# Kernel tuning notes

Hardware: AMD Instinct MI355X
Metric: run time of the kernel (lower is better)

The kernel has to match this reference:

```python
import jax, jax.numpy as jnp
import numpy as np


def setup_inputs() -> dict:
    key = jax.random.key(0)
    ks = jax.random.split(key, 8)
    B = 65536
    x = jax.random.normal(ks[0], (B, 784), dtype=jnp.float32)
    conv_w = jnp.ones((3, 3), dtype=jnp.float32)  # Parameter(ones((3,3)))
    # Linear layers stored as (in, out) weight + (out,) bias
    def lin(k, fin, fout):
        kw, kb = jax.random.split(k)
        bound = 1.0 / np.sqrt(fin)
        W = jax.random.uniform(kw, (fin, fout), minval=-bound, maxval=bound, dtype=jnp.float32)
        b = jax.random.uniform(kb, (fout,), minval=-bound, maxval=bound, dtype=jnp.float32)
        return W, b
    W1, b1 = lin(ks[1], 26 * 26, 500)
    W2, b2 = lin(ks[2], 500, 200)
    W3, b3 = lin(ks[3], 200, 10)
    return {"x": x, "conv_w": conv_w, "W1": W1, "b1": b1,
            "W2": W2, "b2": b2, "W3": W3, "b3": b3}


def reference(x, conv_w, W1, b1, W2, b2, W3, b3):
    B = x.shape[0]
    img = x.reshape(B, 1, 28, 28)  # NCHW, single channel
    kern = conv_w.reshape(1, 1, 3, 3)  # OIHW
    # valid 2D cross-correlation == torch tensordot sliding-window loop
    conv = jax.lax.conv_general_dilated(
        img, kern, window_strides=(1, 1), padding='VALID',
        dimension_numbers=('NCHW', 'OIHW', 'NCHW'))  # (B,1,26,26)
    h = conv.reshape(B, 26 * 26)
    h = jax.nn.relu(h @ W1 + b1)
    h = jax.nn.relu(h @ W2 + b2)
    return h @ W3 + b3  # (B, 10) logits
```

## Files before the change

### kernel.cpp

```cpp
#include <hip/hip_runtime.h>
#include <hip/hip_bf16.h>
#include <stdint.h>

typedef __bf16 bf16x8 __attribute__((ext_vector_type(8)));
typedef float  f32x4  __attribute__((ext_vector_type(4)));


#define KT1 25
#define NF1 32
#define KT2 16
#define NF2 16
#define KT3 8

__global__ void prep_w1(const float* __restrict__ W1, const float* __restrict__ cw,
                        __bf16* __restrict__ w1s) {
  int gid  = blockIdx.x * 256 + threadIdx.x;
  int lane = gid & 63;
  int slot = gid >> 6;
  int t = slot >> 5;
  int f = slot & 31;
  int kbase = t * 32 + ((lane >> 4) << 3);
  int n = f * 16 + (lane & 15);
  float c[9];
#pragma unroll
  for (int i = 0; i < 9; ++i) c[i] = cw[i];
  bf16x8 v;
#pragma unroll
  for (int e = 0; e < 8; ++e) {
    int k = kbase + e;
    float acc = 0.f;
    if (k < 784 && n < 500) {
      int pi = k / 28, pj = k % 28;
#pragma unroll
      for (int dr = 0; dr < 3; ++dr) {
        int r = pi - dr;
        if (r < 0 || r >= 26) continue;
#pragma unroll
        for (int dc = 0; dc < 3; ++dc) {
          int cc = pj - dc;
          if (cc < 0 || cc >= 26) continue;
          acc += c[dr * 3 + dc] * W1[(size_t)(r * 26 + cc) * 500 + n];
        }
      }
    }
    v[e] = (__bf16)acc;
  }
  *(bf16x8*)(w1s + (size_t)(slot * 64 + lane) * 8) = v;
}

__global__ void prep_w2(const float* __restrict__ W2, __bf16* __restrict__ w2s) {
  int gid  = blockIdx.x * 256 + threadIdx.x;
  int lane = gid & 63;
  int slot = gid >> 6;
  int t = slot >> 4;
  int f = slot & 15;
  int kbase = t * 32 + ((lane >> 4) << 3);
  int n = f * 16 + (lane & 15);
  bf16x8 v;
#pragma unroll
  for (int e = 0; e < 8; ++e) {
    int k = kbase + e;
    float val = (k < 500 && n < 200) ? W2[(size_t)k * 200 + n] : 0.f;
    v[e] = (__bf16)val;
  }
  *(bf16x8*)(w2s + (size_t)(slot * 64 + lane) * 8) = v;
}

__global__ void prep_w3(const float* __restrict__ W3, __bf16* __restrict__ w3s) {
  int gid  = blockIdx.x * 256 + threadIdx.x;
  int lane = gid & 63;
  int t    = gid >> 6;
  int kbase = t * 32 + ((lane >> 4) << 3);
  int n = lane & 15;
  bf16x8 v;
#pragma unroll
  for (int e = 0; e < 8; ++e) {
    int k = kbase + e;
    float val = (k < 200 && n < 10) ? W3[(size_t)k * 10 + n] : 0.f;
    v[e] = (__bf16)val;
  }
  *(bf16x8*)(w3s + (size_t)(t * 64 + lane) * 8) = v;
}

__global__ __launch_bounds__(256, 2) void mlp_fused(
    const float* __restrict__ x,
    const __bf16* __restrict__ w1s, const __bf16* __restrict__ w2s,
    const __bf16* __restrict__ w3s,
    const float* __restrict__ b1, const float* __restrict__ b2,
    const float* __restrict__ b3,
    float* __restrict__ out)
{
  __shared__ __align__(16) char xsm[2 * 4096];
  __shared__ __align__(16) char h1[64 * 1024];
  __shared__ float sb1[512];
  __shared__ float sb2[256];

  const int tid  = threadIdx.x;
  const int lane = tid & 63;
  const int w    = tid >> 6;
  const int lrow = lane & 15;
  const int lgrp = lane >> 4;
  const int brow = blockIdx.x * 64;
  const int xr   = tid >> 2;
  const int xq   = tid & 3;

  sb1[tid]       = (tid < 500) ? b1[tid] : 0.f;
  sb1[tid + 256] = (tid + 256 < 500) ? b1[tid + 256] : 0.f;
  sb2[tid]       = (tid < 200) ? b2[tid] : 0.f;

  const f32x4 FZ = {0.f, 0.f, 0.f, 0.f};

  f32x4 acc1[4][8];
#pragma unroll
  for (int m = 0; m < 4; ++m)
#pragma unroll
    for (int f = 0; f < 8; ++f) acc1[m][f] = FZ;

  const bf16x8* w1p   = (const bf16x8*)w1s + ((size_t)(w * 8) * 64 + lane);
  const float*  xbase = x + (size_t)(brow + xr) * 784;
  const int     xoff  = xr * 64 + ((xq ^ (xr & 3)) << 4);

  auto gload = [&](int t, f32x4 (&g)[2]) {
    int gk = t * 32 + xq * 8;
    if (gk > 776) gk = 776;
    const float* p = xbase + gk;
    g[0] = *(const f32x4*)p;
    g[1] = *(const f32x4*)(p + 4);
  };
  auto cwrite = [&](f32x4 (&g)[2], int bw) {
    bf16x8 v;
#pragma unroll
    for (int e = 0; e < 4; ++e) { v[e] = (__bf16)g[0][e]; v[e + 4] = (__bf16)g[1][e]; }
    *(bf16x8*)(xsm + bw + xoff) = v;
  };

  f32x4  grA[2], grB[2];
  bf16x8 bA[8], bB[8];

  auto body1 = [&](int t, bf16x8 (&bc)[8], bf16x8 (&bn)[8],
                   f32x4 (&gc)[2], f32x4 (&gl)[2], int bufR, int bufW) {
    bf16x8 afr[4];
#pragma unroll
    for (int m = 0; m < 4; ++m) {
      int r = m * 16 + lrow;
      afr[m] = *(const bf16x8*)(xsm + bufR + r * 64 + ((lgrp ^ (r & 3)) << 4));
    }
#pragma unroll
    for (int f = 0; f < 8; ++f) bn[f] = w1p[(size_t)((t + 1) * NF1 + f) * 64];
    gload(t + 2 > 24 ? 24 : t + 2, gl);
    cwrite(gc, bufW);

    __builtin_amdgcn_s_setprio(1);
#pragma unroll
    for (int f = 0; f < 8; ++f)
#pragma unroll
      for (int m = 0; m < 4; ++m)
        acc1[m][f] = __builtin_amdgcn_mfma_f32_16x16x32_bf16(afr[m], bc[f], acc1[m][f], 0, 0, 0);
    __builtin_amdgcn_s_setprio(0);

    asm volatile("s_waitcnt lgkmcnt(0)\n\ts_barrier" ::: "memory");
  };

  gload(0, grA);
#pragma unroll
  for (int f = 0; f < 8; ++f) bA[f] = w1p[(size_t)f * 64];
  gload(1, grB);
  cwrite(grA, 0);
  asm volatile("s_waitcnt lgkmcnt(0)\n\ts_barrier" ::: "memory");

  for (int t = 0; t < 24; t += 2) {
    body1(t,     bA, bB, grB, grA, 0,    4096);
    body1(t + 1, bB, bA, grA, grB, 4096, 0);
  }
  {
    bf16x8 afr[4];
#pragma unroll
    for (int m = 0; m < 4; ++m) {
      int r = m * 16 + lrow;
      afr[m] = *(const bf16x8*)(xsm + r * 64 + ((lgrp ^ (r & 3)) << 4));
    }
    __builtin_amdgcn_s_setprio(1);
#pragma unroll
    for (int f = 0; f < 8; ++f)
#pragma unroll
      for (int m = 0; m < 4; ++m)
        acc1[m][f] = __builtin_amdgcn_mfma_f32_16x16x32_bf16(afr[m], bA[f], acc1[m][f], 0, 0, 0);
    __builtin_amdgcn_s_setprio(0);
  }

#pragma unroll
  for (int m = 0; m < 4; ++m) {
#pragma unroll
    for (int f = 0; f < 8; ++f) {
      int col = w * 128 + f * 16 + lrow;
      float bias = sb1[col];
#pragma unroll
      for (int r = 0; r < 4; ++r) {
        int row = m * 16 + lgrp * 4 + r;
        float v = fmaxf(acc1[m][f][r] + bias, 0.f);
        int off = row * 1024 + ((col * 2) ^ ((row & 7) << 4));
        *(__bf16*)(h1 + off) = (__bf16)v;
      }
    }
  }

  const bf16x8* w2p = (const bf16x8*)w2s + ((size_t)(w * 4) * 64 + lane);
  bf16x8 bX[2][4], bY[2][4];
#pragma unroll
  for (int f = 0; f < 4; ++f) bX[0][f] = w2p[(size_t)(0 * NF2 + f) * 64];
#pragma unroll
  for (int f = 0; f < 4; ++f) bX[1][f] = w2p[(size_t)(1 * NF2 + f) * 64];

  asm volatile("s_waitcnt lgkmcnt(0)\n\ts_barrier" ::: "memory");

  f32x4 acc2[4][4];
#pragma unroll
  for (int m = 0; m < 4; ++m)
#pragma unroll
    for (int f = 0; f < 4; ++f) acc2[m][f] = FZ;

  auto pair2 = [&](int tt, bf16x8 (&cur)[2][4], bf16x8 (&nxt)[2][4]) {
#pragma unroll
    for (int f = 0; f < 4; ++f) nxt[0][f] = w2p[(size_t)((tt + 2) * NF2 + f) * 64];
#pragma unroll
    for (int f = 0; f < 4; ++f) nxt[1][f] = w2p[(size_t)((tt + 3) * NF2 + f) * 64];
    {
      bf16x8 a2[4];
#pragma unroll
      for (int m = 0; m < 4; ++m) {
        int row = m * 16 + lrow;
        int off = row * 1024 + ((tt * 64 + lgrp * 16) ^ ((row & 7) << 4));
        a2[m] = *(const bf16x8*)(h1 + off);
      }
      __builtin_amdgcn_s_setprio(1);
#pragma unroll
      for (int f = 0; f < 4; ++f)
#pragma unroll
        for (int m = 0; m < 4; ++m)
          acc2[m][f] = __builtin_amdgcn_mfma_f32_16x16x32_bf16(a2[m], cur[0][f], acc2[m][f], 0, 0, 0);
      __builtin_amdgcn_s_setprio(0);
    }
    {
      bf16x8 a2[4];
#pragma unroll
      for (int m = 0; m < 4; ++m) {
        int row = m * 16 + lrow;
        int off = row * 1024 + (((tt + 1) * 64 + lgrp * 16) ^ ((row & 7) << 4));
        a2[m] = *(const bf16x8*)(h1 + off);
      }
      __builtin_amdgcn_s_setprio(1);
#pragma unroll
      for (int f = 0; f < 4; ++f)
#pragma unroll
        for (int m = 0; m < 4; ++m)
          acc2[m][f] = __builtin_amdgcn_mfma_f32_16x16x32_bf16(a2[m], cur[1][f], acc2[m][f], 0, 0, 0);
      __builtin_amdgcn_s_setprio(0);
    }
  };

  for (int t = 0; t < KT2; t += 4) {
    pair2(t,     bX, bY);
    pair2(t + 2, bY, bX);
  }

  asm volatile("s_waitcnt lgkmcnt(0)\n\ts_barrier" ::: "memory");

#pragma unroll
  for (int m = 0; m < 4; ++m) {
#pragma unroll
    for (int f = 0; f < 4; ++f) {
      int col = w * 64 + f * 16 + lrow;
      float bias = sb2[col];
#pragma unroll
      for (int r = 0; r < 4; ++r) {
        int row = m * 16 + lgrp * 4 + r;
        float v = fmaxf(acc2[m][f][r] + bias, 0.f);
        int off = row * 512 + ((col * 2) ^ ((row & 7) << 4));
        *(__bf16*)(h1 + off) = (__bf16)v;
      }
    }
  }

  const bf16x8* w3p = (const bf16x8*)w3s + lane;
  bf16x8 w3f[8];
#pragma unroll
  for (int t = 0; t < KT3; ++t) w3f[t] = w3p[(size_t)t * 64];

  asm volatile("s_waitcnt lgkmcnt(0)\n\ts_barrier" ::: "memory");

  {
    f32x4 a3 = FZ;
#pragma unroll
    for (int t = 0; t < KT3; ++t) {
      int row = w * 16 + lrow;
      int off = row * 512 + ((t * 64 + lgrp * 16) ^ ((row & 7) << 4));
      bf16x8 a = *(const bf16x8*)(h1 + off);
      a3 = __builtin_amdgcn_mfma_f32_16x16x32_bf16(a, w3f[t], a3, 0, 0, 0);
    }
    if (lrow < 10) {
      float bias = b3[lrow];
#pragma unroll
      for (int r = 0; r < 4; ++r)
        out[(size_t)(brow + w * 16 + lgrp * 4 + r) * 10 + lrow] = a3[r] + bias;
    }
  }
}

extern "C" void kernel_launch(void* const* d_in, const int* in_sizes, int n_in,
                              void* d_out, int out_size, void* d_ws, size_t ws_size,
                              hipStream_t stream) {
  const float* x  = (const float*)d_in[0];
  const float* cw = (const float*)d_in[1];
  const float* W1 = (const float*)d_in[2];
  const float* b1 = (const float*)d_in[3];
  const float* W2 = (const float*)d_in[4];
  const float* b2 = (const float*)d_in[5];
  const float* W3 = (const float*)d_in[6];
  const float* b3 = (const float*)d_in[7];
  float* out = (float*)d_out;

  __bf16* w1s = (__bf16*)d_ws;
  __bf16* w2s = w1s + (size_t)KT1 * NF1 * 64 * 8;
  __bf16* w3s = w2s + (size_t)KT2 * NF2 * 64 * 8;

  prep_w1<<<200, 256, 0, stream>>>(W1, cw, w1s);
  prep_w2<<<64, 256, 0, stream>>>(W2, w2s);
  prep_w3<<<2, 256, 0, stream>>>(W3, w3s);

  mlp_fused<<<65536 / 64, 256, 0, stream>>>(x, w1s, w2s, w3s, b1, b2, b3, out);
}
```

Before: 93.71 us.

## Split fused MLP into two kernels with global h1 staging

Splits the fused three-layer kernel into gemm1, which computes layer 1 split across two N-halves per row tile, and gemm23, which computes layers 2 and 3 and reads h1 from a global workspace in MFMA fragment layout. The aim is to drop the 64KB shared h1 buffer and halve the accumulator count so occupancy can rise to 3 blocks per CU and layer-1 parallelism doubles. The cost is a global round-trip of h1 (about 64MB of bf16) and the x tile being read twice, once per N-half. The work is chunked to fit the workspace size.

```diff
diff --git a/kernel.cpp b/kernel.cpp
--- a/kernel.cpp
+++ b/kernel.cpp
@@ -82,41 +82,39 @@
   *(bf16x8*)(w3s + (size_t)(t * 64 + lane) * 8) = v;
 }
 
-__global__ __launch_bounds__(256, 2) void mlp_fused(
+__global__ __launch_bounds__(256, 3) void gemm1(
     const float* __restrict__ x,
-    const __bf16* __restrict__ w1s, const __bf16* __restrict__ w2s,
-    const __bf16* __restrict__ w3s,
-    const float* __restrict__ b1, const float* __restrict__ b2,
-    const float* __restrict__ b3,
-    float* __restrict__ out)
+    const __bf16* __restrict__ w1s,
+    const float* __restrict__ b1,
+    __bf16* __restrict__ h1f,
+    int mtiles)
 {
   __shared__ __align__(16) char xsm[2 * 4096];
-  __shared__ __align__(16) char h1[64 * 1024];
-  __shared__ float sb1[512];
-  __shared__ float sb2[256];
+  __shared__ __align__(16) char ts[16 * 528];
+  __shared__ float sb1[256];
 
   const int tid  = threadIdx.x;
   const int lane = tid & 63;
   const int w    = tid >> 6;
   const int lrow = lane & 15;
   const int lgrp = lane >> 4;
-  const int brow = blockIdx.x * 64;
+  const int bid  = blockIdx.x;
+  const int nh   = (bid >= mtiles) ? 1 : 0;
+  const int mt   = nh ? bid - mtiles : bid;
+  const int brow = mt * 64;
   const int xr   = tid >> 2;
   const int xq   = tid & 3;
 
-  sb1[tid]       = (tid < 500) ? b1[tid] : 0.f;
-  sb1[tid + 256] = (tid + 256 < 500) ? b1[tid + 256] : 0.f;
-  sb2[tid]       = (tid < 200) ? b2[tid] : 0.f;
+  { int n = nh * 256 + tid; sb1[tid] = (n < 500) ? b1[n] : 0.f; }
 
   const f32x4 FZ = {0.f, 0.f, 0.f, 0.f};
-
-  f32x4 acc1[4][8];
+  f32x4 acc[4][4];
 #pragma unroll
   for (int m = 0; m < 4; ++m)
 #pragma unroll
-    for (int f = 0; f < 8; ++f) acc1[m][f] = FZ;
-
-  const bf16x8* w1p   = (const bf16x8*)w1s + ((size_t)(w * 8) * 64 + lane);
+    for (int f = 0; f < 4; ++f) acc[m][f] = FZ;
+
+  const bf16x8* w1p   = (const bf16x8*)w1s + ((size_t)(nh * 16 + w * 4) * 64 + lane);
   const float*  xbase = x + (size_t)(brow + xr) * 784;
   const int     xoff  = xr * 64 + ((xq ^ (xr & 3)) << 4);
 
@@ -135,9 +133,9 @@
   };
 
   f32x4  grA[2], grB[2];
-  bf16x8 bA[8], bB[8];
-
-  auto body1 = [&](int t, bf16x8 (&bc)[8], bf16x8 (&bn)[8],
+  bf16x8 bA[4], bB[4];
+
+  auto body1 = [&](int t, bf16x8 (&bc)[4], bf16x8 (&bn)[4],
                    f32x4 (&gc)[2], f32x4 (&gl)[2], int bufR, int bufW) {
     bf16x8 afr[4];
 #pragma unroll
@@ -146,16 +144,16 @@
       afr[m] = *(const bf16x8*)(xsm + bufR + r * 64 + ((lgrp ^ (r & 3)) << 4));
     }
 #pragma unroll
-    for (int f = 0; f < 8; ++f) bn[f] = w1p[(size_t)((t + 1) * NF1 + f) * 64];
+    for (int f = 0; f < 4; ++f) bn[f] = w1p[(size_t)((t + 1) * NF1 + f) * 64];
     gload(t + 2 > 24 ? 24 : t + 2, gl);
     cwrite(gc, bufW);
 
     __builtin_amdgcn_s_setprio(1);
 #pragma unroll
-    for (int f = 0; f < 8; ++f)
+    for (int f = 0; f < 4; ++f)
 #pragma unroll
       for (int m = 0; m < 4; ++m)
-        acc1[m][f] = __builtin_amdgcn_mfma_f32_16x16x32_bf16(afr[m], bc[f], acc1[m][f], 0, 0, 0);
+        acc[m][f] = __builtin_amdgcn_mfma_f32_16x16x32_bf16(afr[m], bc[f], acc[m][f], 0, 0, 0);
     __builtin_amdgcn_s_setprio(0);
 
     asm volatile("s_waitcnt lgkmcnt(0)\n\ts_barrier" ::: "memory");
@@ -163,7 +161,7 @@
 
   gload(0, grA);
 #pragma unroll
-  for (int f = 0; f < 8; ++f) bA[f] = w1p[(size_t)f * 64];
+  for (int f = 0; f < 4; ++f) bA[f] = w1p[(size_t)f * 64];
   gload(1, grB);
   cwrite(grA, 0);
   asm volatile("s_waitcnt lgkmcnt(0)\n\ts_barrier" ::: "memory");
@@ -181,89 +179,110 @@
     }
     __builtin_amdgcn_s_setprio(1);
 #pragma unroll
-    for (int f = 0; f < 8; ++f)
+    for (int f = 0; f < 4; ++f)
 #pragma unroll
       for (int m = 0; m < 4; ++m)
-        acc1[m][f] = __builtin_amdgcn_mfma_f32_16x16x32_bf16(afr[m], bA[f], acc1[m][f], 0, 0, 0);
+        acc[m][f] = __builtin_amdgcn_mfma_f32_16x16x32_bf16(afr[m], bA[f], acc[m][f], 0, 0, 0);
     __builtin_amdgcn_s_setprio(0);
   }
+  asm volatile("s_waitcnt lgkmcnt(0)\n\ts_barrier" ::: "memory");
 
 #pragma unroll
   for (int m = 0; m < 4; ++m) {
 #pragma unroll
-    for (int f = 0; f < 8; ++f) {
-      int col = w * 128 + f * 16 + lrow;
+    for (int f = 0; f < 4; ++f) {
+      int col = w * 64 + f * 16 + lrow;
       float bias = sb1[col];
 #pragma unroll
       for (int r = 0; r < 4; ++r) {
-        int row = m * 16 + lgrp * 4 + r;
-        float v = fmaxf(acc1[m][f][r] + bias, 0.f);
-        int off = row * 1024 + ((col * 2) ^ ((row & 7) << 4));
-        *(__bf16*)(h1 + off) = (__bf16)v;
+        int row = lgrp * 4 + r;
+        float v = fmaxf(acc[m][f][r] + bias, 0.f);
+        *(__bf16*)(ts + row * 528 + col * 2) = (__bf16)v;
       }
     }
-  }
-
-  const bf16x8* w2p = (const bf16x8*)w2s + ((size_t)(w * 4) * 64 + lane);
-  bf16x8 bX[2][4], bY[2][4];
-#pragma unroll
-  for (int f = 0; f < 4; ++f) bX[0][f] = w2p[(size_t)(0 * NF2 + f) * 64];
-#pragma unroll
-  for (int f = 0; f < 4; ++f) bX[1][f] = w2p[(size_t)(1 * NF2 + f) * 64];
-
-  asm volatile("s_waitcnt lgkmcnt(0)\n\ts_barrier" ::: "memory");
-
-  f32x4 acc2[4][4];
+    asm volatile("s_waitcnt lgkmcnt(0)\n\ts_barrier" ::: "memory");
+#pragma unroll
+    for (int it = 0; it < 2; ++it) {
+      int s    = it * 256 + tid;
+      int ktl  = s >> 6;
+      int ln   = s & 63;
+      f32x4 v = *(const f32x4*)(ts + (ln & 15) * 528 + (ktl * 32 + (ln >> 4) * 8) * 2);
+      *(f32x4*)((char*)h1f + (((size_t)(mt * 4 + m) * 16) + (nh * 8 + ktl)) * 1024 + ln * 16) = v;
+    }
+    asm volatile("s_waitcnt lgkmcnt(0) vmcnt(0)\n\ts_barrier" ::: "memory");
+  }
+}
+
+__global__ __launch_bounds__(256, 3) void gemm23(
+    const __bf16* __restrict__ h1f,
+    const __bf16* __restrict__ w2s, const __bf16* __restrict__ w3s,
+    const float* __restrict__ b2, const float* __restrict__ b3,
+    float* __restrict__ out)
+{
+  __shared__ __align__(16) char h2s[64 * 512];
+  __shared__ float sb2[256];
+
+  const int tid  = threadIdx.x;
+  const int lane = tid & 63;
+  const int w    = tid >> 6;
+  const int lrow = lane & 15;
+  const int lgrp = lane >> 4;
+  const int brow = blockIdx.x * 64;
+
+  sb2[tid] = (tid < 200) ? b2[tid] : 0.f;
+
+  const f32x4 FZ = {0.f, 0.f, 0.f, 0.f};
+  f32x4 acc[4][4];
 #pragma unroll
   for (int m = 0; m < 4; ++m)
 #pragma unroll
-    for (int f = 0; f < 4; ++f) acc2[m][f] = FZ;
-
-  auto pair2 = [&](int tt, bf16x8 (&cur)[2][4], bf16x8 (&nxt)[2][4]) {
-#pragma unroll
-    for (int f = 0; f < 4; ++f) nxt[0][f] = w2p[(size_t)((tt + 2) * NF2 + f) * 64];
-#pragma unroll
-    for (int f = 0; f < 4; ++f) nxt[1][f] = w2p[(size_t)((tt + 3) * NF2 + f) * 64];
+    for (int f = 0; f < 4; ++f) acc[m][f] = FZ;
+
+  const bf16x8* ap  = (const bf16x8*)h1f + ((size_t)blockIdx.x * 4 * 16) * 64 + lane;
+  const bf16x8* w2p = (const bf16x8*)w2s + ((size_t)(w * 4)) * 64 + lane;
+
+  bf16x8 aP[4], aQ[4], bP[4], bQ[4];
+#pragma unroll
+  for (int m = 0; m < 4; ++m) aP[m] = ap[(size_t)(m * 16 + 0) * 64];
+#pragma unroll
+  for (int f = 0; f < 4; ++f) bP[f] = w2p[(size_t)(0 * NF2 + f) * 64];
+#pragma unroll
+  for (int m = 0; m < 4; ++m) aQ[m] = ap[(size_t)(m * 16 + 1) * 64];
+#pragma unroll
+  for (int f = 0; f < 4; ++f) bQ[f] = w2p[(size_t)(1 * NF2 + f) * 64];
+
+  for (int kt = 0; kt < KT2; kt += 2) {
+    __builtin_amdgcn_s_setprio(1);
+#pragma unroll
+    for (int f = 0; f < 4; ++f)
+#pragma unroll
+      for (int m = 0; m < 4; ++m)
+        acc[m][f] = __builtin_amdgcn_mfma_f32_16x16x32_bf16(aP[m], bP[f], acc[m][f], 0, 0, 0);
+    __builtin_amdgcn_s_setprio(0);
     {
-      bf16x8 a2[4];
-#pragma unroll
-      for (int m = 0; m < 4; ++m) {
-        int row = m * 16 + lrow;
-        int off = row * 1024 + ((tt * 64 + lgrp * 16) ^ ((row & 7) << 4));
-        a2[m] = *(const bf16x8*)(h1 + off);
-      }
-      __builtin_amdgcn_s_setprio(1);
-#pragma unroll
-      for (int f = 0; f < 4; ++f)
-#pragma unroll
-        for (int m = 0; m < 4; ++m)
-          acc2[m][f] = __builtin_amdgcn_mfma_f32_16x16x32_bf16(a2[m], cur[0][f], acc2[m][f], 0, 0, 0);
-      __builtin_amdgcn_s_setprio(0);
-    }
+      int ka = (kt + 2 < 16) ? kt + 2 : 15;
+#pragma unroll
+      for (int m = 0; m < 4; ++m) aP[m] = ap[(size_t)(m * 16 + ka) * 64];
+#pragma unroll
+      for (int f = 0; f < 4; ++f) bP[f] = w2p[(size_t)((kt + 2) * NF2 + f) * 64];
+    }
+    __builtin_amdgcn_s_setprio(1);
+#pragma unroll
+    for (int f = 0; f < 4; ++f)
+#pragma unroll
+      for (int m = 0; m < 4; ++m)
+        acc[m][f] = __builtin_amdgcn_mfma_f32_16x16x32_bf16(aQ[m], bQ[f], acc[m][f], 0, 0, 0);
+    __builtin_amdgcn_s_setprio(0);
     {
-      bf16x8 a2[4];
-#pragma unroll
-      for (int m = 0; m < 4; ++m) {
-        int row = m * 16 + lrow;
-        int off = row * 1024 + (((tt + 1) * 64 + lgrp * 16) ^ ((row & 7) << 4));
-        a2[m] = *(const bf16x8*)(h1 + off);
-      }
-      __builtin_amdgcn_s_setprio(1);
-#pragma unroll
-      for (int f = 0; f < 4; ++f)
-#pragma unroll
-        for (int m = 0; m < 4; ++m)
-          acc2[m][f] = __builtin_amdgcn_mfma_f32_16x16x32_bf16(a2[m], cur[1][f], acc2[m][f], 0, 0, 0);
-      __builtin_amdgcn_s_setprio(0);
-    }
-  };
-
-  for (int t = 0; t < KT2; t += 4) {
-    pair2(t,     bX, bY);
-    pair2(t + 2, bY, bX);
-  }
-
-  asm volatile("s_waitcnt lgkmcnt(0)\n\ts_barrier" ::: "memory");
+      int ka = (kt + 3 < 16) ? kt + 3 : 15;
+#pragma unroll
+      for (int m = 0; m < 4; ++m) aQ[m] = ap[(size_t)(m * 16 + ka) * 64];
+#pragma unroll
+      for (int f = 0; f < 4; ++f) bQ[f] = w2p[(size_t)((kt + 3) * NF2 + f) * 64];
+    }
+  }
+
+  __syncthreads();
 
 #pragma unroll
   for (int m = 0; m < 4; ++m) {
@@ -274,9 +293,9 @@
 #pragma unroll
       for (int r = 0; r < 4; ++r) {
         int row = m * 16 + lgrp * 4 + r;
-        float v = fmaxf(acc2[m][f][r] + bias, 0.f);
+        float v = fmaxf(acc[m][f][r] + bias, 0.f);
         int off = row * 512 + ((col * 2) ^ ((row & 7) << 4));
-        *(__bf16*)(h1 + off) = (__bf16)v;
+        *(__bf16*)(h2s + off) = (__bf16)v;
       }
     }
   }
@@ -294,7 +313,7 @@
     for (int t = 0; t < KT3; ++t) {
       int row = w * 16 + lrow;
       int off = row * 512 + ((t * 64 + lgrp * 16) ^ ((row & 7) << 4));
-      bf16x8 a = *(const bf16x8*)(h1 + off);
+      bf16x8 a = *(const bf16x8*)(h2s + off);
       a3 = __builtin_amdgcn_mfma_f32_16x16x32_bf16(a, w3f[t], a3, 0, 0, 0);
     }
     if (lrow < 10) {
@@ -323,9 +342,22 @@
   __bf16* w2s = w1s + (size_t)KT1 * NF1 * 64 * 8;
   __bf16* w3s = w2s + (size_t)KT2 * NF2 * 64 * 8;
 
+  size_t woff  = ((size_t)KT1 * NF1 + KT2 * NF2 + KT3) * 64 * 8 * sizeof(__bf16);
+  size_t h1off = (woff + 255) & ~(size_t)255;
+  __bf16* h1f  = (__bf16*)((char*)d_ws + h1off);
+
+  size_t avail   = (ws_size > h1off) ? ws_size - h1off : 0;
+  size_t maxrows = avail / 1024;
+  int chunk = 65536;
+  while ((size_t)chunk > maxrows && chunk > 64) chunk >>= 1;
+
   prep_w1<<<200, 256, 0, stream>>>(W1, cw, w1s);
   prep_w2<<<64, 256, 0, stream>>>(W2, w2s);
   prep_w3<<<2, 256, 0, stream>>>(W3, w3s);
 
-  mlp_fused<<<65536 / 64, 256, 0, stream>>>(x, w1s, w2s, w3s, b1, b2, b3, out);
-}
+  for (int r0 = 0; r0 < 65536; r0 += chunk) {
+    int mt = chunk / 64;
+    gemm1<<<mt * 2, 256, 0, stream>>>(x + (size_t)r0 * 784, w1s, b1, h1f, mt);
+    gemm23<<<mt, 256, 0, stream>>>(h1f, w2s, w3s, b2, b3, out + (size_t)r0 * 10);
+  }
+}
```

New measurement: 147.6 us. 57.5% more time.
